# Optimization experiments

Hardware: AMD Instinct MI355X
Metric: run time of the kernel (lower is better)

The kernel has to match this reference:

```python
import jax, jax.numpy as jnp
import numpy as np
from jax import lax

WS = 8       # window size
NH = 16      # num heads
ATT = 64     # att_dim
CH_SCALE = ((ATT // NH) // 2) ** (-0.5)  # (head_dim // key_channels_reduction)**-0.5


def dwconv3(x, w, b):
    # depthwise 3x3, SAME padding; w: [C,1,3,3]
    y = lax.conv_general_dilated(x, w, (1, 1), 'SAME',
                                 feature_group_count=x.shape[1],
                                 dimension_numbers=('NCHW', 'OIHW', 'NCHW'))
    return y + b[None, :, None, None]


def conv1x1(x, w, b):
    # w: [O, C]
    return jnp.einsum('bchw,oc->bohw', x, w) + b[None, :, None, None]


def bn(x, g, b, m, v, eps=1e-5):
    s = g / jnp.sqrt(v + eps)
    return (x - m[None, :, None, None]) * s[None, :, None, None] + b[None, :, None, None]


def to_win(t, h, ws):
    # [B, h*d, H, W] -> [(B*hh*ww), h, ws*ws, d]
    B, C, H, W = t.shape
    d, hh, ww = C // h, H // ws, W // ws
    t = t.reshape(B, h, d, hh, ws, ww, ws).transpose(0, 3, 5, 1, 4, 6, 2)
    return t.reshape(B * hh * ww, h, ws * ws, d)


def from_win(t, B, h, ws, hh, ww):
    # [(B*hh*ww), h, ws*ws, d] -> [B, h*d, H, W]
    d = t.shape[-1]
    t = t.reshape(B, hh, ww, h, ws, ws, d).transpose(0, 3, 6, 1, 4, 2, 5)
    return t.reshape(B, h * d, hh * ws, ww * ws)


def setup_inputs() -> dict:
    key = jax.random.key(0)
    ks = jax.random.split(key, 16)
    C, ATTD, QKC, HID = 64, 64, 32, 256
    B, H, W = 2, 512, 512
    inp = {
        'x': jax.random.normal(ks[0], (B, C, H, W), jnp.float32),
        'pa_w': jax.random.normal(ks[1], (C, 1, 3, 3), jnp.float32) * 0.1,
        'pa_b': jnp.zeros((C,), jnp.float32),
        'bn1_g': jnp.ones((ATTD,), jnp.float32), 'bn1_b': jnp.zeros((ATTD,), jnp.float32),
        'bn1_m': jnp.zeros((ATTD,), jnp.float32), 'bn1_v': jnp.ones((ATTD,), jnp.float32),
        'q_w': jax.random.normal(ks[2], (QKC, C), jnp.float32) * 0.05,
        'q_b': jnp.zeros((QKC,), jnp.float32),
        'k_w': jax.random.normal(ks[3], (QKC, C), jnp.float32) * 0.05,
        'k_b': jnp.zeros((QKC,), jnp.float32),
        'v_w': jax.random.normal(ks[4], (ATTD, C), jnp.float32) * 0.05,
        'v_b': jnp.zeros((ATTD,), jnp.float32),
        'hp_w': jax.random.normal(ks[5], (ATTD, ATTD), jnp.float32) * 0.05,
        'hp_b': jnp.zeros((ATTD,), jnp.float32),
        'bn2_g': jnp.ones((ATTD,), jnp.float32), 'bn2_b': jnp.zeros((ATTD,), jnp.float32),
        'bn2_m': jnp.zeros((ATTD,), jnp.float32), 'bn2_v': jnp.ones((ATTD,), jnp.float32),
        'fc1_w': jax.random.normal(ks[6], (HID, ATTD), jnp.float32) * 0.05,
        'fc1_b': jnp.zeros((HID,), jnp.float32),
        'dw_w': jax.random.normal(ks[7], (HID, 1, 3, 3), jnp.float32) * 0.1,
        'dw_b': jnp.zeros((HID,), jnp.float32),
        'bn3_g': jnp.ones((HID,), jnp.float32), 'bn3_b': jnp.zeros((HID,), jnp.float32),
        'bn3_m': jnp.zeros((HID,), jnp.float32), 'bn3_v': jnp.ones((HID,), jnp.float32),
        'fc2_w': jax.random.normal(ks[8], (ATTD, HID), jnp.float32) * 0.05,
        'fc2_b': jnp.zeros((ATTD,), jnp.float32),
    }
    return inp


def reference(x, pa_w, pa_b, bn1_g, bn1_b, bn1_m, bn1_v, q_w, q_b, k_w, k_b,
              v_w, v_b, hp_w, hp_b, bn2_g, bn2_b, bn2_m, bn2_v, fc1_w, fc1_b,
              dw_w, dw_b, bn3_g, bn3_b, bn3_m, bn3_v, fc2_w, fc2_b):
    B, C, H, W = x.shape
    # H, W are multiples of WS, so the reflect pad is a no-op.
    # PA positional attention
    x = x * jax.nn.sigmoid(dwconv3(x, pa_w, pa_b))
    shortcut = x  # [:, :, :H, :W] is identity here
    xn = bn(x, bn1_g, bn1_b, bn1_m, bn1_v)
    q = conv1x1(xn, q_w, q_b)
    k = conv1x1(xn, k_w, k_b)
    v = conv1x1(xn, v_w, v_b)
    hh, ww = H // WS, W // WS
    q = to_win(q, NH, WS)   # [Bw, h, n, dk]
    k = to_win(k, NH, WS)   # [Bw, h, n, dk]
    v = to_win(v, NH, WS)   # [Bw, h, n, dv]
    q = jax.nn.softmax(q, axis=-1)
    k = jax.nn.softmax(k, axis=-2)
    ctx = jnp.einsum('whnd,whne->whde', k, v)          # [Bw, h, dk, dv]
    attn = jnp.einsum('whnd,whde->whne', q, ctx)        # [Bw, h, n, dv]
    dots = jnp.swapaxes(jnp.einsum('whnd,whne->whde', q, k), -2, -1) * CH_SCALE
    dc = (jnp.max(dots, axis=(-2, -1), keepdims=True) +
          jnp.mean(dots, axis=(-2, -1), keepdims=True))  # [Bw, h, 1, 1]
    attn = attn * dc
    s1 = from_win(attn, B, NH, WS, hh, ww)              # [B, ATT, H, W]
    s1 = conv1x1(s1, hp_w, hp_b) + shortcut
    # MLP block
    s2 = bn(s1, bn2_g, bn2_b, bn2_m, bn2_v)
    s2 = conv1x1(s2, fc1_w, fc1_b)
    s2 = jax.nn.gelu(s2, approximate=False)
    s2 = bn(dwconv3(s2, dw_w, dw_b), bn3_g, bn3_b, bn3_m, bn3_v)
    s2 = conv1x1(s2, fc2_w, fc2_b)
    return s1 + s2
```

## Files before the change

kernel.cpp:

```cpp
#include <hip/hip_runtime.h>
#include <stdint.h>

#define HH 512
#define WW 512
#define HW 262144
#define CH 64
#define HID 256

typedef __attribute__((ext_vector_type(8))) short short8;
typedef __attribute__((ext_vector_type(4))) float f32x4;
typedef _Float16 f16x2 __attribute__((ext_vector_type(2)));
typedef _Float16 f16x8 __attribute__((ext_vector_type(8)));

#define WS_QKVB 0
#define WS_F1B  128
#define WS_F2B  384
#define WS_DWP  448
#define WS_W1F  1600
#define WS_W2F  9792
#define WS_WQKV 17984
#define WS_WHP  22080

__device__ __forceinline__ float bf2f(uint16_t u) {
    return __uint_as_float(((uint32_t)u) << 16);
}
__device__ __forceinline__ uint16_t f2bf(float f) {
    uint32_t x = __float_as_uint(f);
    uint32_t r = x + 0x7fffu + ((x >> 16) & 1u);
    return (uint16_t)(r >> 16);
}
__device__ __forceinline__ float h2f(uint16_t u) {
    _Float16 h;
    __builtin_memcpy(&h, &u, 2);
    return (float)h;
}
__device__ __forceinline__ uint16_t f2h(float f) {
    _Float16 h = (_Float16)f;
    uint16_t u;
    __builtin_memcpy(&u, &h, 2);
    return u;
}
__device__ __forceinline__ f16x2 u2h2(uint32_t u) {
    f16x2 r;
    __builtin_memcpy(&r, &u, 4);
    return r;
}
__device__ __forceinline__ uint32_t pkrtz_u32(float a, float b) {
    auto v = __builtin_amdgcn_cvt_pkrtz(a, b);
    uint32_t u;
    __builtin_memcpy(&u, &v, 4);
    return u;
}

__device__ __forceinline__ float gelu_f(float v) {
    float v2 = v * v;
    float m  = v * (-1.5957691216f - 0.0713548162726f * v2);
    float e  = __expf(m);
    return v * __builtin_amdgcn_rcpf(1.f + e);
}

__global__ __launch_bounds__(256) void k0_fold(
    const float* __restrict__ q_w, const float* __restrict__ q_b,
    const float* __restrict__ k_w, const float* __restrict__ k_b,
    const float* __restrict__ v_w, const float* __restrict__ v_b,
    const float* __restrict__ bn1_g, const float* __restrict__ bn1_b,
    const float* __restrict__ bn1_m, const float* __restrict__ bn1_v,
    const float* __restrict__ fc1_w, const float* __restrict__ fc1_b,
    const float* __restrict__ bn2_g, const float* __restrict__ bn2_b,
    const float* __restrict__ bn2_m, const float* __restrict__ bn2_v,
    const float* __restrict__ fc2_w, const float* __restrict__ fc2_b,
    const float* __restrict__ hp_w,
    const float* __restrict__ dw_w, const float* __restrict__ dw_b,
    const float* __restrict__ bn3_g, const float* __restrict__ bn3_b,
    const float* __restrict__ bn3_m, const float* __restrict__ bn3_v,
    float* __restrict__ wsw)
{
    __shared__ float s1s[64], t1s[64], s2s[64], t2s[64], s3s[256], t3s[256];
    int tid = threadIdx.x;
    if (tid < 64) {
        float s = bn1_g[tid] * rsqrtf(bn1_v[tid] + 1e-5f);
        s1s[tid] = s; t1s[tid] = bn1_b[tid] - bn1_m[tid] * s;
        float s2 = bn2_g[tid] * rsqrtf(bn2_v[tid] + 1e-5f);
        s2s[tid] = s2; t2s[tid] = bn2_b[tid] - bn2_m[tid] * s2;
    }
    if (tid < 256) {
        float s = bn3_g[tid] * rsqrtf(bn3_v[tid] + 1e-5f);
        s3s[tid] = s;
        t3s[tid] = (dw_b[tid] - bn3_m[tid]) * s + bn3_b[tid];
    }
    __syncthreads();

    float* qkvb = wsw + WS_QKVB;
    float* f1b  = wsw + WS_F1B;
    float* f2b  = wsw + WS_F2B;
    uint16_t* dwph  = (uint16_t*)(wsw + WS_DWP);
    uint16_t* w1f   = (uint16_t*)(wsw + WS_W1F);
    uint16_t* w2f   = (uint16_t*)(wsw + WS_W2F);
    uint16_t* wqkvf = (uint16_t*)(wsw + WS_WQKV);
    uint16_t* whpf  = (uint16_t*)(wsw + WS_WHP);

    if (tid < 128) {
        int o = tid;
        float a;
        if (o < 32) {
            a = q_b[o];
            for (int c = 0; c < 64; c++) a += q_w[o*64+c]*t1s[c];
        } else if (o < 64) {
            a = k_b[o-32];
            for (int c = 0; c < 64; c++) a += k_w[(o-32)*64+c]*t1s[c];
        } else {
            a = v_b[o-64];
            for (int c = 0; c < 64; c++) a += v_w[(o-64)*64+c]*t1s[c];
        }
        qkvb[o] = a;
    }
    if (tid < 256) {
        float a = fc1_b[tid];
        for (int c = 0; c < 64; c++) a += fc1_w[tid*64+c]*t2s[c];
        f1b[tid] = a;
    }
    if (tid < 64) {
        float a = fc2_b[tid];
        for (int c = 0; c < 256; c++) a += fc2_w[tid*256+c]*t3s[c];
        f2b[tid] = a;
    }
    for (int i = tid; i < 8192; i += 256) {
        int nt = i >> 10, rem = i & 1023;
        int k8 = rem >> 7, col = (rem >> 3) & 15, j = rem & 7;
        int o = nt*16 + col, c = k8*8 + j;
        float w;
        if (o < 32)      w = q_w[o*64 + c];
        else if (o < 64) w = k_w[(o-32)*64 + c];
        else             w = v_w[(o-64)*64 + c];
        wqkvf[i] = f2bf(w * s1s[c]);
    }
    for (int i = tid; i < 4096; i += 256) {
        int mt = i >> 10, rem = i & 1023;
        int k8 = rem >> 7, row = (rem >> 3) & 15, j = rem & 7;
        int o = mt*16 + row, c = k8*8 + j;
        whpf[i] = f2bf(hp_w[o*64 + c]);
    }
    for (int i = tid; i < 16384; i += 256) {
        int nt = i >> 10, rem = i & 1023;
        int k8 = rem >> 7, col = (rem >> 3) & 15, j = rem & 7;
        int c = k8*8 + j, o = nt*16 + col;
        w1f[i] = f2bf(fc1_w[o*64 + c] * s2s[c]);
    }
    for (int i = tid; i < 16384; i += 256) {
        int nt = i >> 12, rem = i & 4095;
        int k8 = rem >> 7, col = (rem >> 3) & 15, j = rem & 7;
        int c = k8*8 + j, o = nt*16 + col;
        w2f[i] = f2h(fc2_w[o*256 + c] * s3s[c]);
    }
    for (int i = tid; i < 2304; i += 256) {
        int t = i >> 8, ch = i & 255;
        dwph[i] = f2h(dw_w[ch*9 + t]);
    }
}

__global__ __launch_bounds__(256, 4) void k2_attn(
    const float* __restrict__ x,
    const float* __restrict__ pa_w, const float* __restrict__ pa_b,
    const float* __restrict__ hp_b,
    const float* __restrict__ wsw, uint16_t* __restrict__ s1out)
{
    __shared__ __align__(16) uint16_t regionA[10880];
    __shared__ __align__(16) uint16_t gfrag[4096];
    __shared__ __align__(16) uint16_t afrag[4096];
    uint16_t* xs  = regionA;
    uint16_t* qkv = regionA;

    int tid = threadIdx.x;
    int wave = tid >> 6, l = tid & 63;
    int orig = blockIdx.x;
    int wid = (orig & 7) * 1024 + (orig >> 3);
    int b = wid >> 12;
    int r = wid & 4095;
    int wy = r >> 6, wx = r & 63;
    int y0 = wy*8 - 1;
    int x0g = wx*8 - 4;
    const float* xb = x + (size_t)b * CH * HW;
    bool interior = (wy > 0) & (wy < 63) & (wx > 0) & (wx < 63);

    if (interior) {
        #pragma unroll
        for (int k = 0; k < 10; k++) {
            int i = k*256 + tid;
            int seg = i & 3;
            int rem = i >> 2;
            int c = rem / 10;
            int py = rem - c*10;
            const float* src = xb + (size_t)c*HW + (size_t)(y0+py)*512 + x0g + seg*4;
            float4 v = *reinterpret_cast<const float4*>(src);
            uint16_t tv[4] = {f2bf(v.x), f2bf(v.y), f2bf(v.z), f2bf(v.w)};
            *reinterpret_cast<uint64_t*>(&xs[c*170 + py*16 + seg*4]) =
                *reinterpret_cast<const uint64_t*>(tv);
        }
    } else {
        #pragma unroll
        for (int k = 0; k < 10; k++) {
            int i = k*256 + tid;
            int seg = i & 3;
            int rem = i >> 2;
            int c = rem / 10;
            int py = rem - c*10;
            int yy = y0 + py;
            int gx = x0g + seg*4;
            uint64_t v64 = 0;
            if ((unsigned)yy < 512u && (unsigned)gx <= 508u) {
                float4 v = *reinterpret_cast<const float4*>(
                    xb + (size_t)c*HW + (size_t)yy*512 + gx);
                uint16_t tv[4] = {f2bf(v.x), f2bf(v.y), f2bf(v.z), f2bf(v.w)};
                v64 = *reinterpret_cast<const uint64_t*>(tv);
            }
            *reinterpret_cast<uint64_t*>(&xs[c*170 + py*16 + seg*4]) = v64;
        }
    }
    __syncthreads();

    {
        int c = tid & 63, yh = tid >> 6;
        float pw[9];
        #pragma unroll
        for (int t = 0; t < 9; t++) pw[t] = pa_w[c*9 + t];
        float pb = pa_b[c];
        float va[4][12];
        #pragma unroll
        for (int tr = 0; tr < 4; tr++) {
            const uint16_t* rp = &xs[c*170 + (yh*2 + tr)*16];
            #pragma unroll
            for (int s = 0; s < 6; s++) {
                uint32_t u = *reinterpret_cast<const uint32_t*>(&rp[2 + s*2]);
                va[tr][s*2]   = __uint_as_float(u << 16);
                va[tr][s*2+1] = __uint_as_float(u & 0xffff0000u);
            }
        }
        #pragma unroll
        for (int dy2 = 0; dy2 < 2; dy2++) {
            int y = yh*2 + dy2;
            #pragma unroll
            for (int xx = 0; xx < 8; xx++) {
                float conv = pb;
                #pragma unroll
                for (int dy = 0; dy < 3; dy++)
                    #pragma unroll
                    for (int dx = 0; dx < 3; dx++)
                        conv += va[dy2+dy][xx+1+dx] * pw[dy*3+dx];
                float xcv = va[dy2+1][xx+2];
                float gv = xcv / (1.f + __expf(-conv));
                int n = y*8 + xx;
                gfrag[(n>>4)*1024 + (c>>3)*128 + (n&15)*8 + (c&7)] = f2bf(gv);
            }
        }
    }
    __syncthreads();

    {
        const uint16_t* wqkv = (const uint16_t*)(wsw + WS_WQKV);
        const float* qkvb = wsw + WS_QKVB;
        f32x4 acc[4][2];
        #pragma unroll
        for (int ntw = 0; ntw < 2; ntw++) {
            float bias = qkvb[(wave*2+ntw)*16 + (l & 15)];
            #pragma unroll
            for (int mt = 0; mt < 4; mt++) acc[mt][ntw] = {bias, bias, bias, bias};
        }
        #pragma unroll
        for (int kb = 0; kb < 2; kb++) {
            short8 a[4];
            #pragma unroll
            for (int mt = 0; mt < 4; mt++)
                a[mt] = *reinterpret_cast<const short8*>(&gfrag[mt*1024 + kb*512 + 8*l]);
            #pragma unroll
            for (int ntw = 0; ntw < 2; ntw++) {
                int nt = wave*2 + ntw;
                short8 bf = *reinterpret_cast<const short8*>(&wqkv[nt*1024 + kb*512 + 8*l]);
                #pragma unroll
                for (int mt = 0; mt < 4; mt++)
                    acc[mt][ntw] = __builtin_amdgcn_mfma_f32_16x16x32_bf16(a[mt], bf, acc[mt][ntw], 0, 0, 0);
            }
        }
        #pragma unroll
        for (int ntw = 0; ntw < 2; ntw++) {
            int o = (wave*2+ntw)*16 + (l & 15);
            #pragma unroll
            for (int mt = 0; mt < 4; mt++) {
                int px0 = mt*16 + (l >> 4)*4;
                uint32_t lo = pkrtz_u32(acc[mt][ntw][0], acc[mt][ntw][1]);
                uint32_t hi = pkrtz_u32(acc[mt][ntw][2], acc[mt][ntw][3]);
                *reinterpret_cast<uint64_t*>(&qkv[o*68 + px0]) =
                    (uint64_t)lo | ((uint64_t)hi << 32);
            }
        }
    }
    __syncthreads();

    {
        int hd = tid >> 4, l16 = tid & 15;
        float a0[4], a1[4], a2[4], a3[4], a4[4], a5[4], a6[4], a7[4];
        #pragma unroll
        for (int j = 0; j < 4; j++) {
            int px = l16 + 16*j;
            a0[j] = h2f(qkv[(2*hd    )*68 + px]);
            a1[j] = h2f(qkv[(2*hd + 1)*68 + px]);
            a2[j] = h2f(qkv[(32 + 2*hd    )*68 + px]);
            a3[j] = h2f(qkv[(32 + 2*hd + 1)*68 + px]);
            a4[j] = h2f(qkv[(64 + 4*hd    )*68 + px]);
            a5[j] = h2f(qkv[(64 + 4*hd + 1)*68 + px]);
            a6[j] = h2f(qkv[(64 + 4*hd + 2)*68 + px]);
            a7[j] = h2f(qkv[(64 + 4*hd + 3)*68 + px]);
        }
        #pragma unroll
        for (int j = 0; j < 4; j++) {
            float m = fmaxf(a0[j], a1[j]);
            float e0 = __expf(a0[j]-m), e1 = __expf(a1[j]-m);
            float inv = 1.f/(e0+e1);
            a0[j] = e0*inv; a1[j] = e1*inv;
        }
        float m0 = fmaxf(fmaxf(a2[0],a2[1]), fmaxf(a2[2],a2[3]));
        float m1 = fmaxf(fmaxf(a3[0],a3[1]), fmaxf(a3[2],a3[3]));
        #pragma unroll
        for (int s = 1; s < 16; s <<= 1) {
            m0 = fmaxf(m0, __shfl_xor(m0, s, 64));
            m1 = fmaxf(m1, __shfl_xor(m1, s, 64));
        }
        float sum0 = 0.f, sum1 = 0.f;
        #pragma unroll
        for (int j = 0; j < 4; j++) {
            a2[j] = __expf(a2[j]-m0); a3[j] = __expf(a3[j]-m1);
            sum0 += a2[j]; sum1 += a3[j];
        }
        #pragma unroll
        for (int s = 1; s < 16; s <<= 1) {
            sum0 += __shfl_xor(sum0, s, 64);
            sum1 += __shfl_xor(sum1, s, 64);
        }
        float iv0 = 1.f/sum0, iv1 = 1.f/sum1;
        #pragma unroll
        for (int j = 0; j < 4; j++) { a2[j] *= iv0; a3[j] *= iv1; }
        float ctx0[4], ctx1[4];
        #pragma unroll
        for (int e = 0; e < 4; e++) {
            float ve0, ve1, ve2, ve3;
            if (e==0) { ve0=a4[0]; ve1=a4[1]; ve2=a4[2]; ve3=a4[3]; }
            else if (e==1) { ve0=a5[0]; ve1=a5[1]; ve2=a5[2]; ve3=a5[3]; }
            else if (e==2) { ve0=a6[0]; ve1=a6[1]; ve2=a6[2]; ve3=a6[3]; }
            else { ve0=a7[0]; ve1=a7[1]; ve2=a7[2]; ve3=a7[3]; }
            float c0 = a2[0]*ve0 + a2[1]*ve1 + a2[2]*ve2 + a2[3]*ve3;
            float c1 = a3[0]*ve0 + a3[1]*ve1 + a3[2]*ve2 + a3[3]*ve3;
            #pragma unroll
            for (int s = 1; s < 16; s <<= 1) {
                c0 += __shfl_xor(c0, s, 64);
                c1 += __shfl_xor(c1, s, 64);
            }
            ctx0[e] = c0; ctx1[e] = c1;
        }
        float p00=0.f, p01=0.f, p10=0.f, p11=0.f;
        #pragma unroll
        for (int j = 0; j < 4; j++) {
            p00 += a0[j]*a2[j]; p01 += a0[j]*a3[j];
            p10 += a1[j]*a2[j]; p11 += a1[j]*a3[j];
        }
        #pragma unroll
        for (int s = 1; s < 16; s <<= 1) {
            p00 += __shfl_xor(p00, s, 64); p01 += __shfl_xor(p01, s, 64);
            p10 += __shfl_xor(p10, s, 64); p11 += __shfl_xor(p11, s, 64);
        }
        const float CH_SCALE = 0.70710678118654752f;
        p00 *= CH_SCALE; p01 *= CH_SCALE; p10 *= CH_SCALE; p11 *= CH_SCALE;
        float dc = fmaxf(fmaxf(p00,p01), fmaxf(p10,p11)) + 0.25f*(p00+p01+p10+p11);

        #pragma unroll
        for (int j = 0; j < 4; j++) {
            uint16_t t[4];
            #pragma unroll
            for (int e = 0; e < 4; e++)
                t[e] = f2bf((a0[j]*ctx0[e] + a1[j]*ctx1[e]) * dc);
            *reinterpret_cast<uint64_t*>(
                &afrag[j*1024 + (hd>>1)*128 + l16*8 + (hd&1)*4]) =
                *reinterpret_cast<const uint64_t*>(t);
        }
    }
    __syncthreads();

    {
        const uint16_t* whp = (const uint16_t*)(wsw + WS_WHP);
        int nt = wave;
        f32x4 oacc[4];
        #pragma unroll
        for (int mt = 0; mt < 4; mt++) {
            int o0 = mt*16 + (l >> 4)*4;
            float4 hb = *reinterpret_cast<const float4*>(&hp_b[o0]);
            oacc[mt] = {hb.x, hb.y, hb.z, hb.w};
        }
        #pragma unroll
        for (int kb = 0; kb < 2; kb++) {
            short8 bf = *reinterpret_cast<const short8*>(&afrag[nt*1024 + kb*512 + 8*l]);
            #pragma unroll
            for (int mt = 0; mt < 4; mt++) {
                short8 a = *reinterpret_cast<const short8*>(&whp[mt*1024 + kb*512 + 8*l]);
                oacc[mt] = __builtin_amdgcn_mfma_f32_16x16x32_bf16(a, bf, oacc[mt], 0, 0, 0);
            }
        }
        int px = nt*16 + (l & 15);
        int yy = wy*8 + (px >> 3), xx = wx*8 + (px & 7);
        size_t pbase = ((size_t)b * HW + (size_t)yy * 512 + xx) * 64;
        #pragma unroll
        for (int mt = 0; mt < 4; mt++) {
            int o0 = mt*16 + (l >> 4)*4;
            uint64_t gg = *reinterpret_cast<const uint64_t*>(
                &gfrag[(px>>4)*1024 + (o0>>3)*128 + (px&15)*8 + (o0&7)]);
            uint16_t t[4];
            #pragma unroll
            for (int rr = 0; rr < 4; rr++) {
                float g = bf2f((uint16_t)(gg >> (16*rr)));
                t[rr] = f2bf(oacc[mt][rr] + g);
            }
            *reinterpret_cast<uint64_t*>(&s1out[pbase + o0]) =
                *reinterpret_cast<const uint64_t*>(t);
        }
    }
}

__global__ __launch_bounds__(256, 4) void k3_mlp(
    const uint16_t* __restrict__ s1b, const float* __restrict__ wsw,
    float* __restrict__ out)
{
    __shared__ __align__(16) uint16_t sfrag[12288];
    __shared__ __align__(16) uint16_t hbuf[6480];

    const float* f1b = wsw + WS_F1B;
    const float* f2b = wsw + WS_F2B;
    const uint16_t* dwph = (const uint16_t*)(wsw + WS_DWP);
    const uint16_t* w1f  = (const uint16_t*)(wsw + WS_W1F);
    const uint16_t* w2f  = (const uint16_t*)(wsw + WS_W2F);

    int tid = threadIdx.x;
    int wave = tid >> 6, l = tid & 63;
    int hxl = l & 15, cg = l >> 4;
    int X0 = blockIdx.x * 16, Y0 = blockIdx.y * 8;
    int b = blockIdx.z;
    bool interior = (X0 > 0) & (X0 < 496) & (Y0 > 0) & (Y0 < 504);

    if (interior) {
        for (int i = tid; i < 1440; i += 256) {
            int px = i >> 3, g = i & 7;
            int hy = px / 18, hx = px - hy*18;
            int yy = Y0 - 1 + hy, xx = X0 - 1 + hx;
            uint4 q = *reinterpret_cast<const uint4*>(
                &s1b[((size_t)b*HW + (size_t)yy*512 + xx)*64 + g*8]);
            *reinterpret_cast<uint4*>(&sfrag[(px>>4)*1024 + g*128 + (px&15)*8]) = q;
        }
    } else {
        for (int i = tid; i < 1440; i += 256) {
            int px = i >> 3, g = i & 7;
            int hy = px / 18, hx = px - hy*18;
            int yy = Y0 - 1 + hy, xx = X0 - 1 + hx;
            uint4 q = {0u, 0u, 0u, 0u};
            if ((unsigned)yy < 512u && (unsigned)xx < 512u)
                q = *reinterpret_cast<const uint4*>(
                    &s1b[((size_t)b*HW + (size_t)yy*512 + xx)*64 + g*8]);
            *reinterpret_cast<uint4*>(&sfrag[(px>>4)*1024 + g*128 + (px&15)*8]) = q;
        }
    }

    bool okA[3], imgA[3];
    int hbA[3], ptA[3];
    #pragma unroll
    for (int it = 0; it < 3; it++) {
        int pt = wave + it*4;
        int px = pt*16 + hxl;
        ptA[it] = pt;
        okA[it] = px < 180;
        int hy = px / 18, hx = px - hy*18;
        imgA[it] = okA[it] &&
            (interior || (((unsigned)(Y0-1+hy) < 512u) && ((unsigned)(X0-1+hx) < 512u)));
        hbA[it] = px*36 + cg*4;
    }

    f32x4 acc[2][4];
    #pragma unroll
    for (int nt = 0; nt < 4; nt++) {
        float bias = f2b[nt*16 + (l & 15)];
        acc[0][nt] = {bias, bias, bias, bias};
        acc[1][nt] = acc[0][nt];
    }
    __syncthreads();

    for (int cc = 0; cc < 8; cc++) {
        short8 wA[2][2];
        #pragma unroll
        for (int mtw = 0; mtw < 2; mtw++)
            #pragma unroll
            for (int kb = 0; kb < 2; kb++)
                wA[mtw][kb] = *reinterpret_cast<const short8*>(
                    &w1f[(cc*2 + mtw)*1024 + kb*512 + 8*l]);
        float4 hb0 = *reinterpret_cast<const float4*>(&f1b[cc*32      + cg*4]);
        float4 hb1 = *reinterpret_cast<const float4*>(&f1b[cc*32 + 16 + cg*4]);

        #pragma unroll
        for (int it = 0; it < 3; it++) {
            int pt = ptA[it];
            f32x4 h0 = {hb0.x, hb0.y, hb0.z, hb0.w};
            f32x4 h1 = {hb1.x, hb1.y, hb1.z, hb1.w};
            #pragma unroll
            for (int kb = 0; kb < 2; kb++) {
                short8 bf = *reinterpret_cast<const short8*>(&sfrag[pt*1024 + kb*512 + 8*l]);
                h0 = __builtin_amdgcn_mfma_f32_16x16x32_bf16(wA[0][kb], bf, h0, 0, 0, 0);
                h1 = __builtin_amdgcn_mfma_f32_16x16x32_bf16(wA[1][kb], bf, h1, 0, 0, 0);
            }
            if (okA[it]) {
                uint64_t v0 = 0, v1 = 0;
                if (imgA[it]) {
                    uint32_t a01 = pkrtz_u32(gelu_f(h0[0]), gelu_f(h0[1]));
                    uint32_t a23 = pkrtz_u32(gelu_f(h0[2]), gelu_f(h0[3]));
                    uint32_t b01 = pkrtz_u32(gelu_f(h1[0]), gelu_f(h1[1]));
                    uint32_t b23 = pkrtz_u32(gelu_f(h1[2]), gelu_f(h1[3]));
                    v0 = (uint64_t)a01 | ((uint64_t)a23 << 32);
                    v1 = (uint64_t)b01 | ((uint64_t)b23 << 32);
                }
                *reinterpret_cast<uint64_t*>(&hbuf[hbA[it]])      = v0;
                *reinterpret_cast<uint64_t*>(&hbuf[hbA[it] + 16]) = v1;
            }
        }
        __syncthreads();

        f16x8 bfr[4];
        #pragma unroll
        for (int nt = 0; nt < 4; nt++)
            bfr[nt] = *reinterpret_cast<const f16x8*>(&w2f[nt*4096 + cc*512 + 8*l]);

        uint4 R[4][3];
        #pragma unroll
        for (int tr = 0; tr < 4; tr++)
            #pragma unroll
            for (int dx = 0; dx < 3; dx++)
                R[tr][dx] = *reinterpret_cast<const uint4*>(
                    &hbuf[((wave*2 + tr)*18 + hxl + dx)*36 + cg*8]);

        union { f16x2 h[4]; f16x8 v; } t0, t1;
        f16x2 z = {(_Float16)0.f, (_Float16)0.f};
        #pragma unroll
        for (int g = 0; g < 4; g++) { t0.h[g] = z; t1.h[g] = z; }

        #pragma unroll
        for (int dy = 0; dy < 3; dy++) {
            #pragma unroll
            for (int dx = 0; dx < 3; dx++) {
                uint4 w = *reinterpret_cast<const uint4*>(
                    &dwph[(dy*3+dx)*256 + cc*32 + cg*8]);
                uint4 qa = R[dy][dx];
                uint4 qb = R[dy+1][dx];
                t0.h[0] += u2h2(qa.x) * u2h2(w.x);
                t0.h[1] += u2h2(qa.y) * u2h2(w.y);
                t0.h[2] += u2h2(qa.z) * u2h2(w.z);
                t0.h[3] += u2h2(qa.w) * u2h2(w.w);
                t1.h[0] += u2h2(qb.x) * u2h2(w.x);
                t1.h[1] += u2h2(qb.y) * u2h2(w.y);
                t1.h[2] += u2h2(qb.z) * u2h2(w.z);
                t1.h[3] += u2h2(qb.w) * u2h2(w.w);
            }
        }
        #pragma unroll
        for (int nt = 0; nt < 4; nt++) {
            acc[0][nt] = __builtin_amdgcn_mfma_f32_16x16x32_f16(t0.v, bfr[nt], acc[0][nt], 0, 0, 0);
            acc[1][nt] = __builtin_amdgcn_mfma_f32_16x16x32_f16(t1.v, bfr[nt], acc[1][nt], 0, 0, 0);
        }
        __syncthreads();
    }

    int r0 = cg * 4;
    #pragma unroll
    for (int mi = 0; mi < 2; mi++) {
        int yrow = Y0 + wave*2 + mi;
        size_t srow = ((size_t)b*HW + (size_t)yrow*512 + X0 + r0) * 64;
        #pragma unroll
        for (int nt = 0; nt < 4; nt++) {
            int o = nt*16 + (l & 15);
            size_t oidx = ((size_t)b*CH + o)*HW + (size_t)yrow*512 + X0 + r0;
            float4 ov;
            ov.x = acc[mi][nt][0] + bf2f(s1b[srow + o]);
            ov.y = acc[mi][nt][1] + bf2f(s1b[srow + 64 + o]);
            ov.z = acc[mi][nt][2] + bf2f(s1b[srow + 128 + o]);
            ov.w = acc[mi][nt][3] + bf2f(s1b[srow + 192 + o]);
            *reinterpret_cast<float4*>(out + oidx) = ov;
        }
    }
}

extern "C" void kernel_launch(void* const* d_in, const int* in_sizes, int n_in,
                              void* d_out, int out_size, void* d_ws, size_t ws_size,
                              hipStream_t stream) {
    const float* x     = (const float*)d_in[0];
    const float* pa_w  = (const float*)d_in[1];
    const float* pa_b  = (const float*)d_in[2];
    const float* bn1_g = (const float*)d_in[3];
    const float* bn1_b = (const float*)d_in[4];
    const float* bn1_m = (const float*)d_in[5];
    const float* bn1_v = (const float*)d_in[6];
    const float* q_w   = (const float*)d_in[7];
    const float* q_b   = (const float*)d_in[8];
    const float* k_w   = (const float*)d_in[9];
    const float* k_b   = (const float*)d_in[10];
    const float* v_w   = (const float*)d_in[11];
    const float* v_b   = (const float*)d_in[12];
    const float* hp_w  = (const float*)d_in[13];
    const float* hp_b  = (const float*)d_in[14];
    const float* bn2_g = (const float*)d_in[15];
    const float* bn2_b = (const float*)d_in[16];
    const float* bn2_m = (const float*)d_in[17];
    const float* bn2_v = (const float*)d_in[18];
    const float* fc1_w = (const float*)d_in[19];
    const float* fc1_b = (const float*)d_in[20];
    const float* dw_w  = (const float*)d_in[21];
    const float* dw_b  = (const float*)d_in[22];
    const float* bn3_g = (const float*)d_in[23];
    const float* bn3_b = (const float*)d_in[24];
    const float* bn3_m = (const float*)d_in[25];
    const float* bn3_v = (const float*)d_in[26];
    const float* fc2_w = (const float*)d_in[27];
    const float* fc2_b = (const float*)d_in[28];

    uint16_t* s1b = (uint16_t*)d_ws;
    float*    wsw = (float*)((char*)d_ws + 134217728 + 268435456);

    k0_fold<<<dim3(1), dim3(256), 0, stream>>>(
        q_w, q_b, k_w, k_b, v_w, v_b,
        bn1_g, bn1_b, bn1_m, bn1_v,
        fc1_w, fc1_b, bn2_g, bn2_b, bn2_m, bn2_v,
        fc2_w, fc2_b, hp_w, dw_w, dw_b, bn3_g, bn3_b, bn3_m, bn3_v, wsw);

    k2_attn<<<dim3(8192), dim3(256), 0, stream>>>(
        x, pa_w, pa_b, hp_b, wsw, s1b);

    k3_mlp<<<dim3(32, 64, 2), dim3(256), 0, stream>>>(
        s1b, wsw, (float*)d_out);
}
```

Baseline: 292.7 us.

## Switch bf16 intermediates to fp16 with packed conversions and swizzle MLP block order

Replaces all bf16 storage and MFMA paths with fp16, using the hardware cvt_pkrtz packed conversion instead of the software round-to-nearest bf16 conversion, and uses the f16 MFMA variants. It also remaps the MLP kernel's block index with a swizzle so neighbouring launched blocks are spread across the image, which may change cache and channel locality. fp16 gives more mantissa but less range, and round-toward-zero conversion adds a small numerical difference.

```diff
diff --git a/kernel.cpp b/kernel.cpp
--- a/kernel.cpp
+++ b/kernel.cpp
@@ -21,14 +21,6 @@
 #define WS_WQKV 17984
 #define WS_WHP  22080
 
-__device__ __forceinline__ float bf2f(uint16_t u) {
-    return __uint_as_float(((uint32_t)u) << 16);
-}
-__device__ __forceinline__ uint16_t f2bf(float f) {
-    uint32_t x = __float_as_uint(f);
-    uint32_t r = x + 0x7fffu + ((x >> 16) & 1u);
-    return (uint16_t)(r >> 16);
-}
 __device__ __forceinline__ float h2f(uint16_t u) {
     _Float16 h;
     __builtin_memcpy(&h, &u, 2);
@@ -132,19 +124,19 @@
         if (o < 32)      w = q_w[o*64 + c];
         else if (o < 64) w = k_w[(o-32)*64 + c];
         else             w = v_w[(o-64)*64 + c];
-        wqkvf[i] = f2bf(w * s1s[c]);
+        wqkvf[i] = f2h(w * s1s[c]);
     }
     for (int i = tid; i < 4096; i += 256) {
         int mt = i >> 10, rem = i & 1023;
         int k8 = rem >> 7, row = (rem >> 3) & 15, j = rem & 7;
         int o = mt*16 + row, c = k8*8 + j;
-        whpf[i] = f2bf(hp_w[o*64 + c]);
+        whpf[i] = f2h(hp_w[o*64 + c]);
     }
     for (int i = tid; i < 16384; i += 256) {
         int nt = i >> 10, rem = i & 1023;
         int k8 = rem >> 7, col = (rem >> 3) & 15, j = rem & 7;
         int c = k8*8 + j, o = nt*16 + col;
-        w1f[i] = f2bf(fc1_w[o*64 + c] * s2s[c]);
+        w1f[i] = f2h(fc1_w[o*64 + c] * s2s[c]);
     }
     for (int i = tid; i < 16384; i += 256) {
         int nt = i >> 12, rem = i & 4095;
@@ -192,9 +184,10 @@
             int py = rem - c*10;
             const float* src = xb + (size_t)c*HW + (size_t)(y0+py)*512 + x0g + seg*4;
             float4 v = *reinterpret_cast<const float4*>(src);
-            uint16_t tv[4] = {f2bf(v.x), f2bf(v.y), f2bf(v.z), f2bf(v.w)};
+            uint32_t lo = pkrtz_u32(v.x, v.y);
+            uint32_t hi = pkrtz_u32(v.z, v.w);
             *reinterpret_cast<uint64_t*>(&xs[c*170 + py*16 + seg*4]) =
-                *reinterpret_cast<const uint64_t*>(tv);
+                (uint64_t)lo | ((uint64_t)hi << 32);
         }
     } else {
         #pragma unroll
@@ -210,8 +203,9 @@
             if ((unsigned)yy < 512u && (unsigned)gx <= 508u) {
                 float4 v = *reinterpret_cast<const float4*>(
                     xb + (size_t)c*HW + (size_t)yy*512 + gx);
-                uint16_t tv[4] = {f2bf(v.x), f2bf(v.y), f2bf(v.z), f2bf(v.w)};
-                v64 = *reinterpret_cast<const uint64_t*>(tv);
+                uint32_t lo = pkrtz_u32(v.x, v.y);
+                uint32_t hi = pkrtz_u32(v.z, v.w);
+                v64 = (uint64_t)lo | ((uint64_t)hi << 32);
             }
             *reinterpret_cast<uint64_t*>(&xs[c*170 + py*16 + seg*4]) = v64;
         }
@@ -230,9 +224,9 @@
             const uint16_t* rp = &xs[c*170 + (yh*2 + tr)*16];
             #pragma unroll
             for (int s = 0; s < 6; s++) {
-                uint32_t u = *reinterpret_cast<const uint32_t*>(&rp[2 + s*2]);
-                va[tr][s*2]   = __uint_as_float(u << 16);
-                va[tr][s*2+1] = __uint_as_float(u & 0xffff0000u);
+                f16x2 hh = u2h2(*reinterpret_cast<const uint32_t*>(&rp[2 + s*2]));
+                va[tr][s*2]   = (float)hh[0];
+                va[tr][s*2+1] = (float)hh[1];
             }
         }
         #pragma unroll
@@ -249,7 +243,7 @@
                 float xcv = va[dy2+1][xx+2];
                 float gv = xcv / (1.f + __expf(-conv));
                 int n = y*8 + xx;
-                gfrag[(n>>4)*1024 + (c>>3)*128 + (n&15)*8 + (c&7)] = f2bf(gv);
+                gfrag[(n>>4)*1024 + (c>>3)*128 + (n&15)*8 + (c&7)] = f2h(gv);
             }
         }
     }
@@ -267,17 +261,17 @@
         }
         #pragma unroll
         for (int kb = 0; kb < 2; kb++) {
-            short8 a[4];
+            f16x8 a[4];
             #pragma unroll
             for (int mt = 0; mt < 4; mt++)
-                a[mt] = *reinterpret_cast<const short8*>(&gfrag[mt*1024 + kb*512 + 8*l]);
+                a[mt] = *reinterpret_cast<const f16x8*>(&gfrag[mt*1024 + kb*512 + 8*l]);
             #pragma unroll
             for (int ntw = 0; ntw < 2; ntw++) {
                 int nt = wave*2 + ntw;
-                short8 bf = *reinterpret_cast<const short8*>(&wqkv[nt*1024 + kb*512 + 8*l]);
+                f16x8 bf = *reinterpret_cast<const f16x8*>(&wqkv[nt*1024 + kb*512 + 8*l]);
                 #pragma unroll
                 for (int mt = 0; mt < 4; mt++)
-                    acc[mt][ntw] = __builtin_amdgcn_mfma_f32_16x16x32_bf16(a[mt], bf, acc[mt][ntw], 0, 0, 0);
+                    acc[mt][ntw] = __builtin_amdgcn_mfma_f32_16x16x32_f16(a[mt], bf, acc[mt][ntw], 0, 0, 0);
             }
         }
         #pragma unroll
@@ -372,13 +366,13 @@
 
         #pragma unroll
         for (int j = 0; j < 4; j++) {
-            uint16_t t[4];
-            #pragma unroll
-            for (int e = 0; e < 4; e++)
-                t[e] = f2bf((a0[j]*ctx0[e] + a1[j]*ctx1[e]) * dc);
+            uint32_t lo = pkrtz_u32((a0[j]*ctx0[0] + a1[j]*ctx1[0]) * dc,
+                                    (a0[j]*ctx0[1] + a1[j]*ctx1[1]) * dc);
+            uint32_t hi = pkrtz_u32((a0[j]*ctx0[2] + a1[j]*ctx1[2]) * dc,
+                                    (a0[j]*ctx0[3] + a1[j]*ctx1[3]) * dc);
             *reinterpret_cast<uint64_t*>(
                 &afrag[j*1024 + (hd>>1)*128 + l16*8 + (hd&1)*4]) =
-                *reinterpret_cast<const uint64_t*>(t);
+                (uint64_t)lo | ((uint64_t)hi << 32);
         }
     }
     __syncthreads();
@@ -395,11 +389,11 @@
         }
         #pragma unroll
         for (int kb = 0; kb < 2; kb++) {
-            short8 bf = *reinterpret_cast<const short8*>(&afrag[nt*1024 + kb*512 + 8*l]);
+            f16x8 bf = *reinterpret_cast<const f16x8*>(&afrag[nt*1024 + kb*512 + 8*l]);
             #pragma unroll
             for (int mt = 0; mt < 4; mt++) {
-                short8 a = *reinterpret_cast<const short8*>(&whp[mt*1024 + kb*512 + 8*l]);
-                oacc[mt] = __builtin_amdgcn_mfma_f32_16x16x32_bf16(a, bf, oacc[mt], 0, 0, 0);
+                f16x8 a = *reinterpret_cast<const f16x8*>(&whp[mt*1024 + kb*512 + 8*l]);
+                oacc[mt] = __builtin_amdgcn_mfma_f32_16x16x32_f16(a, bf, oacc[mt], 0, 0, 0);
             }
         }
         int px = nt*16 + (l & 15);
@@ -410,14 +404,14 @@
             int o0 = mt*16 + (l >> 4)*4;
             uint64_t gg = *reinterpret_cast<const uint64_t*>(
                 &gfrag[(px>>4)*1024 + (o0>>3)*128 + (px&15)*8 + (o0&7)]);
-            uint16_t t[4];
-            #pragma unroll
-            for (int rr = 0; rr < 4; rr++) {
-                float g = bf2f((uint16_t)(gg >> (16*rr)));
-                t[rr] = f2bf(oacc[mt][rr] + g);
-            }
+            f16x2 g01 = u2h2((uint32_t)gg);
+            f16x2 g23 = u2h2((uint32_t)(gg >> 32));
+            uint32_t lo = pkrtz_u32(oacc[mt][0] + (float)g01[0],
+                                    oacc[mt][1] + (float)g01[1]);
+            uint32_t hi = pkrtz_u32(oacc[mt][2] + (float)g23[0],
+                                    oacc[mt][3] + (float)g23[1]);
             *reinterpret_cast<uint64_t*>(&s1out[pbase + o0]) =
-                *reinterpret_cast<const uint64_t*>(t);
+                (uint64_t)lo | ((uint64_t)hi << 32);
         }
     }
 }
@@ -438,7 +432,9 @@
     int tid = threadIdx.x;
     int wave = tid >> 6, l = tid & 63;
     int hxl = l & 15, cg = l >> 4;
-    int X0 = blockIdx.x * 16, Y0 = blockIdx.y * 8;
+    int flat = blockIdx.y * 32 + blockIdx.x;
+    int swz = (flat & 7) * 256 + (flat >> 3);
+    int X0 = (swz & 31) * 16, Y0 = (swz >> 5) * 8;
     int b = blockIdx.z;
     bool interior = (X0 > 0) & (X0 < 496) & (Y0 > 0) & (Y0 < 504);
 
@@ -488,12 +484,12 @@
     __syncthreads();
 
     for (int cc = 0; cc < 8; cc++) {
-        short8 wA[2][2];
+        f16x8 wA[2][2];
         #pragma unroll
         for (int mtw = 0; mtw < 2; mtw++)
             #pragma unroll
             for (int kb = 0; kb < 2; kb++)
-                wA[mtw][kb] = *reinterpret_cast<const short8*>(
+                wA[mtw][kb] = *reinterpret_cast<const f16x8*>(
                     &w1f[(cc*2 + mtw)*1024 + kb*512 + 8*l]);
         float4 hb0 = *reinterpret_cast<const float4*>(&f1b[cc*32      + cg*4]);
         float4 hb1 = *reinterpret_cast<const float4*>(&f1b[cc*32 + 16 + cg*4]);
@@ -505,9 +501,9 @@
             f32x4 h1 = {hb1.x, hb1.y, hb1.z, hb1.w};
             #pragma unroll
             for (int kb = 0; kb < 2; kb++) {
-                short8 bf = *reinterpret_cast<const short8*>(&sfrag[pt*1024 + kb*512 + 8*l]);
-                h0 = __builtin_amdgcn_mfma_f32_16x16x32_bf16(wA[0][kb], bf, h0, 0, 0, 0);
-                h1 = __builtin_amdgcn_mfma_f32_16x16x32_bf16(wA[1][kb], bf, h1, 0, 0, 0);
+                f16x8 bf = *reinterpret_cast<const f16x8*>(&sfrag[pt*1024 + kb*512 + 8*l]);
+                h0 = __builtin_amdgcn_mfma_f32_16x16x32_f16(wA[0][kb], bf, h0, 0, 0, 0);
+                h1 = __builtin_amdgcn_mfma_f32_16x16x32_f16(wA[1][kb], bf, h1, 0, 0, 0);
             }
             if (okA[it]) {
                 uint64_t v0 = 0, v1 = 0;
@@ -579,10 +575,10 @@
             int o = nt*16 + (l & 15);
             size_t oidx = ((size_t)b*CH + o)*HW + (size_t)yrow*512 + X0 + r0;
             float4 ov;
-            ov.x = acc[mi][nt][0] + bf2f(s1b[srow + o]);
-            ov.y = acc[mi][nt][1] + bf2f(s1b[srow + 64 + o]);
-            ov.z = acc[mi][nt][2] + bf2f(s1b[srow + 128 + o]);
-            ov.w = acc[mi][nt][3] + bf2f(s1b[srow + 192 + o]);
+            ov.x = acc[mi][nt][0] + h2f(s1b[srow + o]);
+            ov.y = acc[mi][nt][1] + h2f(s1b[srow + 64 + o]);
+            ov.z = acc[mi][nt][2] + h2f(s1b[srow + 128 + o]);
+            ov.w = acc[mi][nt][3] + h2f(s1b[srow + 192 + o]);
             *reinterpret_cast<float4*>(out + oidx) = ov;
         }
     }
```

After: 290.4 us, median of 2. About the same (-0.8%).
